# Kernel tuning notes

Hardware: AMD Instinct MI355X
Metric: run time of the kernel (lower is better)

Reference implementation:

```python
import jax, jax.numpy as jnp
import numpy as np

NUM_USERS = 100000
NUM_ITEMS = 50000
EMB = 64
NNZ = 4_800_000
N = NUM_USERS + NUM_ITEMS


def setup_inputs() -> dict:
    key = jax.random.key(0)
    k1, k2, k3, k4, k5 = jax.random.split(key, 5)
    row = jax.random.randint(k1, (NNZ,), 0, N, dtype=jnp.int64 if jax.config.jax_enable_x64 else jnp.int32)
    col = jax.random.randint(k2, (NNZ,), 0, N, dtype=row.dtype)
    # normalized adjacency values (positive, ~1/avg_degree scale)
    vals = jax.random.uniform(k3, (NNZ,), dtype=jnp.float32) * (1.0 / 32.0)
    user_emb = jax.random.normal(k4, (NUM_USERS, EMB), dtype=jnp.float32)
    item_emb = jax.random.normal(k5, (NUM_ITEMS, EMB), dtype=jnp.float32)
    return {"row": row, "col": col, "vals": vals,
            "user_emb": user_emb, "item_emb": item_emb, "n_layers": 3}


def reference(row, col, vals, user_emb, item_emb, n_layers):
    # ego_embeddings = cat(user, item)  -> [N, D]
    ego = jnp.concatenate([user_emb, item_emb], axis=0)
    acc = ego  # running sum over layers (layer 0 included)
    for _ in range(n_layers):
        # sparse.mm(norm_adj, ego): gather source rows, scale, scatter-add to dest rows
        ego = jax.ops.segment_sum(vals[:, None] * ego[col], row, num_segments=N)
        acc = acc + ego
    mean_emb = acc / jnp.asarray(n_layers + 1, dtype=acc.dtype)  # mean over layer axis
    return mean_emb[:NUM_USERS], mean_emb[NUM_USERS:]
```

## Files before the change

### kernel.cpp

```cpp
#include <hip/hip_runtime.h>
#include <hip/hip_fp16.h>


#define NUSERS 100000
#define NITEMS 50000
#define NN     150000
#define D      64
#define NNZ_E  4800000

#define NB_BU  586
#define BU_PAD 592
#define NCHUNK 256
#define CH     18750
#define STAGE_CAP 16384

__global__ void init_kernel(const float* __restrict__ ue,
                            const float* __restrict__ ie,
                            float* __restrict__ acc,
                            __half* __restrict__ ego) {
    int t = blockIdx.x * blockDim.x + threadIdx.x;
    const int total = NN * (D / 4);
    if (t >= total) return;
    const int user_f4 = NUSERS * (D / 4);
    float4 v;
    if (t < user_f4) v = ((const float4*)ue)[t];
    else             v = ((const float4*)ie)[t - user_f4];
    ((float4*)acc)[t] = v;
    __half2 h01 = __float22half2_rn(make_float2(v.x, v.y));
    __half2 h23 = __float22half2_rn(make_float2(v.z, v.w));
    uint2 packed;
    packed.x = *(unsigned*)&h01;
    packed.y = *(unsigned*)&h23;
    ((uint2*)ego)[t] = packed;
}

__global__ void p1_kernel(const int* __restrict__ row, int* __restrict__ cnt) {
    __shared__ int l[BU_PAD];
    for (int i = threadIdx.x; i < BU_PAD; i += 512) l[i] = 0;
    __syncthreads();
    int b = blockIdx.x;
    int beg = b * CH, end = min(beg + CH, NNZ_E);
    for (int e = beg + threadIdx.x; e < end; e += 512)
        atomicAdd(&l[row[e] >> 8], 1);
    __syncthreads();
    for (int i = threadIdx.x; i < BU_PAD; i += 512) cnt[b * BU_PAD + i] = l[i];
}

__global__ void s1_kernel(const int* __restrict__ cnt,
                          int* __restrict__ woff,
                          int* __restrict__ butot) {
    __shared__ int wsum[4];
    int bu = blockIdx.x;
    int c = threadIdx.x;
    int lane = c & 63;
    int w = c >> 6;
    int d = cnt[c * BU_PAD + bu];
    int incl = d;
    #pragma unroll
    for (int off = 1; off < 64; off <<= 1) {
        int t = __shfl_up(incl, off, 64);
        if (lane >= off) incl += t;
    }
    if (lane == 63) wsum[w] = incl;
    __syncthreads();
    int woffs = 0;
    for (int i = 0; i < w; ++i) woffs += wsum[i];
    woff[c * BU_PAD + bu] = woffs + incl - d;
    if (c == 255) butot[bu] = woffs + incl;
}

__global__ void s2_kernel(const int* __restrict__ butot, int* __restrict__ bbase) {
    __shared__ int sh[1024];
    int t = threadIdx.x;
    sh[t] = (t < NB_BU) ? butot[t] : 0;
    __syncthreads();
    for (int off = 1; off < 1024; off <<= 1) {
        int x = (t >= off) ? sh[t - off] : 0;
        __syncthreads();
        sh[t] += x;
        __syncthreads();
    }
    if (t == 0) bbase[0] = 0;
    if (t < NB_BU) bbase[t + 1] = sh[t];
}

__global__ void p2_kernel(const int* __restrict__ row,
                          const int* __restrict__ col,
                          const float* __restrict__ vals,
                          const int* __restrict__ woff,
                          const int* __restrict__ bbase,
                          uint2* __restrict__ rec) {
    __shared__ int cur[BU_PAD];
    int b = blockIdx.x;
    for (int i = threadIdx.x; i < BU_PAD; i += 512) {
        int base = (i < NB_BU) ? bbase[i] : 0;
        cur[i] = base + woff[b * BU_PAD + i];
    }
    __syncthreads();
    int beg = b * CH, end = min(beg + CH, NNZ_E);
    for (int e = beg + threadIdx.x; e < end; e += 512) {
        int r = row[e];
        unsigned code = (unsigned)(vals[e] * 524288.0f + 0.5f);
        code = min(code, 16383u);
        unsigned cv = ((unsigned)col[e] << 14) | code;
        int p = atomicAdd(&cur[r >> 8], 1);
        rec[p] = make_uint2(cv, (unsigned)(r & 255));
    }
}

__global__ __launch_bounds__(512) void p3f_kernel(const int* __restrict__ bbase,
                                                  const uint2* __restrict__ rec,
                                                  int* __restrict__ start,
                                                  int* __restrict__ deg,
                                                  unsigned* __restrict__ ecv) {
    __shared__ unsigned stage[STAGE_CAP];
    __shared__ int lh[256];
    __shared__ int cur[256];
    __shared__ int wsum[4];
    int bu = blockIdx.x;
    int beg = bbase[bu], end = bbase[bu + 1];
    int t = threadIdx.x;
    if (t < 256) lh[t] = 0;
    __syncthreads();
    for (int i = beg + t; i < end; i += 512)
        atomicAdd(&lh[rec[i].y], 1);
    __syncthreads();
    int h = 0, incl = 0;
    int lane = t & 63, w = t >> 6;
    if (t < 256) {
        h = lh[t];
        incl = h;
        #pragma unroll
        for (int off = 1; off < 64; off <<= 1) {
            int x = __shfl_up(incl, off, 64);
            if (lane >= off) incl += x;
        }
        if (lane == 63) wsum[w] = incl;
    }
    __syncthreads();
    if (t < 256) {
        int woffs = 0;
        for (int i = 0; i < w; ++i) woffs += wsum[i];
        int excl = woffs + incl - h;
        cur[t] = excl;
        int n0 = (bu << 8) + t;
        if (n0 < NN) {
            start[n0] = beg + excl;
            deg[n0] = h;
        }
    }
    __syncthreads();
    for (int i = beg + t; i < end; i += 512) {
        uint2 r = rec[i];
        int p = atomicAdd(&cur[r.y], 1);
        stage[p] = r.x;
    }
    __syncthreads();
    int n_edges = end - beg;
    for (int i = t; i < n_edges; i += 512)
        ecv[beg + i] = stage[i];
}

#define STEP(rj, cj) do {                                              \
    float v_ = (float)((cj) & 16383u) * (1.0f / 524288.0f);            \
    const __half* h_ = (const __half*)&(rj);                           \
    sum[0] = fmaf(v_, __half2float(h_[0]), sum[0]);                    \
    sum[1] = fmaf(v_, __half2float(h_[1]), sum[1]);                    \
    sum[2] = fmaf(v_, __half2float(h_[2]), sum[2]);                    \
    sum[3] = fmaf(v_, __half2float(h_[3]), sum[3]);                    \
    sum[4] = fmaf(v_, __half2float(h_[4]), sum[4]);                    \
    sum[5] = fmaf(v_, __half2float(h_[5]), sum[5]);                    \
    sum[6] = fmaf(v_, __half2float(h_[6]), sum[6]);                    \
    sum[7] = fmaf(v_, __half2float(h_[7]), sum[7]);                    \
} while (0)

__global__ void gather_kernel(const int* __restrict__ start,
                              const int* __restrict__ deg,
                              const unsigned* __restrict__ ecv,
                              const __half* __restrict__ ego,
                              __half* __restrict__ nxt,
                              float* __restrict__ acc,
                              float s, int write_next) {
    int wid = threadIdx.x >> 6;
    int lane = threadIdx.x & 63;
    int n = blockIdx.x * 4 + wid;
    int st = start[n];
    int dg = deg[n];
    int k = lane & 7;
    int g = lane >> 3;
    const float4* ego4 = (const float4*)ego;
    float sum[8] = {0.f, 0.f, 0.f, 0.f, 0.f, 0.f, 0.f, 0.f};

    for (int b = 0; b < dg; b += 64) {
        unsigned cv = (b + lane < dg) ? ecv[st + b + lane] : 0u;

        unsigned c0 = (unsigned)__shfl((int)cv,      g, 64);
        unsigned c1 = (unsigned)__shfl((int)cv,  8 + g, 64);
        unsigned c2 = (unsigned)__shfl((int)cv, 16 + g, 64);
        unsigned c3 = (unsigned)__shfl((int)cv, 24 + g, 64);
        unsigned c4 = (unsigned)__shfl((int)cv, 32 + g, 64);
        unsigned c5 = (unsigned)__shfl((int)cv, 40 + g, 64);
        unsigned c6 = (unsigned)__shfl((int)cv, 48 + g, 64);
        unsigned c7 = (unsigned)__shfl((int)cv, 56 + g, 64);

        float4 r0 = ego4[(c0 >> 14) * 8 + k];
        float4 r1 = ego4[(c1 >> 14) * 8 + k];
        float4 r2 = ego4[(c2 >> 14) * 8 + k];
        float4 r3 = ego4[(c3 >> 14) * 8 + k];
        float4 r4 = ego4[(c4 >> 14) * 8 + k];
        float4 r5 = ego4[(c5 >> 14) * 8 + k];
        float4 r6 = ego4[(c6 >> 14) * 8 + k];
        float4 r7 = ego4[(c7 >> 14) * 8 + k];

        STEP(r0, c0);
        STEP(r1, c1);
        STEP(r2, c2);
        STEP(r3, c3);
        STEP(r4, c4);
        STEP(r5, c5);
        STEP(r6, c6);
        STEP(r7, c7);
    }

    #pragma unroll
    for (int off = 8; off < 64; off <<= 1) {
        #pragma unroll
        for (int i = 0; i < 8; ++i) sum[i] += __shfl_xor(sum[i], off, 64);
    }
    if (g < 2) {
        float4 sv = (g == 0) ? make_float4(sum[0], sum[1], sum[2], sum[3])
                             : make_float4(sum[4], sum[5], sum[6], sum[7]);
        int o = n * 16 + 2 * k + g;
        float4 a = ((float4*)acc)[o];
        a.x = (a.x + sv.x) * s;
        a.y = (a.y + sv.y) * s;
        a.z = (a.z + sv.z) * s;
        a.w = (a.w + sv.w) * s;
        ((float4*)acc)[o] = a;
    }
    if (write_next && g == 0) {
        __half2 h0 = __float22half2_rn(make_float2(sum[0], sum[1]));
        __half2 h1 = __float22half2_rn(make_float2(sum[2], sum[3]));
        __half2 h2 = __float22half2_rn(make_float2(sum[4], sum[5]));
        __half2 h3 = __float22half2_rn(make_float2(sum[6], sum[7]));
        uint4 packed;
        packed.x = *(unsigned*)&h0;
        packed.y = *(unsigned*)&h1;
        packed.z = *(unsigned*)&h2;
        packed.w = *(unsigned*)&h3;
        ((uint4*)nxt)[n * 8 + k] = packed;
    }
}

extern "C" void kernel_launch(void* const* d_in, const int* in_sizes, int n_in,
                              void* d_out, int out_size, void* d_ws, size_t ws_size,
                              hipStream_t stream) {
    const int*   row  = (const int*)d_in[0];
    const int*   col  = (const int*)d_in[1];
    const float* vals = (const float*)d_in[2];
    const float* ue   = (const float*)d_in[3];
    const float* ie   = (const float*)d_in[4];

    float* acc = (float*)d_out;

    char* ws = (char*)d_ws;
    __half*   ego     = (__half*)(ws);
    __half*   nxt     = (__half*)(ws + (size_t)NN * D * 2);
    int*      cnt     = (int*)nxt;
    int*      woff    = cnt + (size_t)NCHUNK * BU_PAD;
    char*     p       = ws + 2 * (size_t)NN * D * 2;
    int*      start   = (int*)(p);              p += (size_t)NN * 4;
    int*      deg     = (int*)(p);              p += (size_t)NN * 4;
    int*      butot   = (int*)(p);              p += BU_PAD * 4;
    int*      bbase   = (int*)(p);              p += (BU_PAD + 8) * 4;
    unsigned* ecv     = (unsigned*)(p);         p += (size_t)NNZ_E * 4;
    uint2*    rec     = (uint2*)(p);

    const int f4_total = NN * (D / 4);
    const int init_blocks = (f4_total + 255) / 256;
    init_kernel<<<init_blocks, 256, 0, stream>>>(ue, ie, acc, ego);

    p1_kernel<<<NCHUNK, 512, 0, stream>>>(row, cnt);
    s1_kernel<<<NB_BU, 256, 0, stream>>>(cnt, woff, butot);
    s2_kernel<<<1, 1024, 0, stream>>>(butot, bbase);
    p2_kernel<<<NCHUNK, 512, 0, stream>>>(row, col, vals, woff, bbase, rec);
    p3f_kernel<<<NB_BU, 512, 0, stream>>>(bbase, rec, start, deg, ecv);

    const int gather_blocks = NN / 4;
    __half* in  = ego;
    __half* out = nxt;
    for (int layer = 0; layer < 3; ++layer) {
        float s = (layer == 2) ? 0.25f : 1.0f;
        int write_next = (layer < 2) ? 1 : 0;
        gather_kernel<<<gather_blocks, 256, 0, stream>>>(start, deg, ecv, in, out, acc,
                                                         s, write_next);
        __half* tmp = in; in = out; out = tmp;
    }
}
```

Measured before the change: 593.5 us.

## Use more, smaller edge chunks for binning and trim padded gather steps

The edge-binning phase now splits the edge list into 1024 chunks of 256 threads instead of 256 chunks of 512 threads. The count-scan kernel is widened to 1024 threads to match, which spreads the histogram and scatter work over more blocks. The gather loop now iterates only over the 8-edge groups that actually exist in each 64-edge batch, two at a time. This avoids wasted loads and FMAs on padding when a node's degree is small (the average is about 32). The trade-off is a larger count/offset table and a dynamic loop with fewer loads in flight per iteration.

Result: faster. 542.9 us (-8.5%).

```diff
diff --git a/kernel.cpp b/kernel.cpp
--- a/kernel.cpp
+++ b/kernel.cpp
@@ -10,8 +10,8 @@
 
 #define NB_BU  586
 #define BU_PAD 592
-#define NCHUNK 256
-#define CH     18750
+#define NCHUNK 1024
+#define CH     4688
 #define STAGE_CAP 16384
 
 __global__ void init_kernel(const float* __restrict__ ue,
@@ -36,20 +36,20 @@
 
 __global__ void p1_kernel(const int* __restrict__ row, int* __restrict__ cnt) {
     __shared__ int l[BU_PAD];
-    for (int i = threadIdx.x; i < BU_PAD; i += 512) l[i] = 0;
+    for (int i = threadIdx.x; i < BU_PAD; i += 256) l[i] = 0;
     __syncthreads();
     int b = blockIdx.x;
     int beg = b * CH, end = min(beg + CH, NNZ_E);
-    for (int e = beg + threadIdx.x; e < end; e += 512)
+    for (int e = beg + threadIdx.x; e < end; e += 256)
         atomicAdd(&l[row[e] >> 8], 1);
     __syncthreads();
-    for (int i = threadIdx.x; i < BU_PAD; i += 512) cnt[b * BU_PAD + i] = l[i];
+    for (int i = threadIdx.x; i < BU_PAD; i += 256) cnt[b * BU_PAD + i] = l[i];
 }
 
 __global__ void s1_kernel(const int* __restrict__ cnt,
                           int* __restrict__ woff,
                           int* __restrict__ butot) {
-    __shared__ int wsum[4];
+    __shared__ int wsum[16];
     int bu = blockIdx.x;
     int c = threadIdx.x;
     int lane = c & 63;
@@ -66,7 +66,7 @@
     int woffs = 0;
     for (int i = 0; i < w; ++i) woffs += wsum[i];
     woff[c * BU_PAD + bu] = woffs + incl - d;
-    if (c == 255) butot[bu] = woffs + incl;
+    if (c == 1023) butot[bu] = woffs + incl;
 }
 
 __global__ void s2_kernel(const int* __restrict__ butot, int* __restrict__ bbase) {
@@ -92,13 +92,13 @@
                           uint2* __restrict__ rec) {
     __shared__ int cur[BU_PAD];
     int b = blockIdx.x;
-    for (int i = threadIdx.x; i < BU_PAD; i += 512) {
+    for (int i = threadIdx.x; i < BU_PAD; i += 256) {
         int base = (i < NB_BU) ? bbase[i] : 0;
         cur[i] = base + woff[b * BU_PAD + i];
     }
     __syncthreads();
     int beg = b * CH, end = min(beg + CH, NNZ_E);
-    for (int e = beg + threadIdx.x; e < end; e += 512) {
+    for (int e = beg + threadIdx.x; e < end; e += 256) {
         int r = row[e];
         unsigned code = (unsigned)(vals[e] * 524288.0f + 0.5f);
         code = min(code, 16383u);
@@ -193,33 +193,17 @@
 
     for (int b = 0; b < dg; b += 64) {
         unsigned cv = (b + lane < dg) ? ecv[st + b + lane] : 0u;
-
-        unsigned c0 = (unsigned)__shfl((int)cv,      g, 64);
-        unsigned c1 = (unsigned)__shfl((int)cv,  8 + g, 64);
-        unsigned c2 = (unsigned)__shfl((int)cv, 16 + g, 64);
-        unsigned c3 = (unsigned)__shfl((int)cv, 24 + g, 64);
-        unsigned c4 = (unsigned)__shfl((int)cv, 32 + g, 64);
-        unsigned c5 = (unsigned)__shfl((int)cv, 40 + g, 64);
-        unsigned c6 = (unsigned)__shfl((int)cv, 48 + g, 64);
-        unsigned c7 = (unsigned)__shfl((int)cv, 56 + g, 64);
-
-        float4 r0 = ego4[(c0 >> 14) * 8 + k];
-        float4 r1 = ego4[(c1 >> 14) * 8 + k];
-        float4 r2 = ego4[(c2 >> 14) * 8 + k];
-        float4 r3 = ego4[(c3 >> 14) * 8 + k];
-        float4 r4 = ego4[(c4 >> 14) * 8 + k];
-        float4 r5 = ego4[(c5 >> 14) * 8 + k];
-        float4 r6 = ego4[(c6 >> 14) * 8 + k];
-        float4 r7 = ego4[(c7 >> 14) * 8 + k];
-
-        STEP(r0, c0);
-        STEP(r1, c1);
-        STEP(r2, c2);
-        STEP(r3, c3);
-        STEP(r4, c4);
-        STEP(r5, c5);
-        STEP(r6, c6);
-        STEP(r7, c7);
+        int m = min(64, dg - b);
+        int steps = (m + 7) >> 3;
+
+        for (int j = 0; j < steps; j += 2) {
+            unsigned ca = (unsigned)__shfl((int)cv, 8 * j + g, 64);
+            unsigned cb = (unsigned)__shfl((int)cv, 8 * j + 8 + g, 64);
+            float4 ra = ego4[(ca >> 14) * 8 + k];
+            float4 rb = ego4[(cb >> 14) * 8 + k];
+            STEP(ra, ca);
+            STEP(rb, cb);
+        }
     }
 
     #pragma unroll
@@ -280,10 +264,10 @@
     const int init_blocks = (f4_total + 255) / 256;
     init_kernel<<<init_blocks, 256, 0, stream>>>(ue, ie, acc, ego);
 
-    p1_kernel<<<NCHUNK, 512, 0, stream>>>(row, cnt);
-    s1_kernel<<<NB_BU, 256, 0, stream>>>(cnt, woff, butot);
+    p1_kernel<<<NCHUNK, 256, 0, stream>>>(row, cnt);
+    s1_kernel<<<NB_BU, 1024, 0, stream>>>(cnt, woff, butot);
     s2_kernel<<<1, 1024, 0, stream>>>(butot, bbase);
-    p2_kernel<<<NCHUNK, 512, 0, stream>>>(row, col, vals, woff, bbase, rec);
+    p2_kernel<<<NCHUNK, 256, 0, stream>>>(row, col, vals, woff, bbase, rec);
     p3f_kernel<<<NB_BU, 512, 0, stream>>>(bbase, rec, start, deg, ecv);
 
     const int gather_blocks = NN / 4;
```
